# Optimization experiments

Measured on AMD Instinct MI355X. Metric: run time of the kernel, lower is better.

The kernel has to match this reference:

```python
import jax, jax.numpy as jnp
import numpy as np

K = 3
STRIDE = 1


def ste_round(v):
    # Round with straight-through gradient (torch Round Function)
    return v + jax.lax.stop_gradient(jnp.round(v) - v)


def ste_sign(v):
    # Sign with straight-through gradient (torch Sign Function)
    return v + jax.lax.stop_gradient(jnp.sign(v) - v)


def _unfold(x, k, s):
    # torch nn.functional.unfold: [B,C,H,W] -> [B, C*k*k, L], channel-major (c, kh, kw)
    B, C, H, W = x.shape
    Ho = (H - k) // s + 1
    Wo = (W - k) // s + 1
    cols = jnp.stack(
        [x[:, :, i:i + s * Ho:s, j:j + s * Wo:s] for i in range(k) for j in range(k)],
        axis=2,
    )  # [B, C, k*k, Ho, Wo]
    return cols.reshape(B, C * k * k, Ho * Wo)


def reference(x, weight, conv_bias, in_min, in_max, prob_table, rand_idx):
    B = x.shape[0]
    O = weight.shape[0]
    cols = _unfold(x, K, STRIDE)                       # [B, CKK, L]
    CKK = cols.shape[1]
    X = cols.transpose(0, 2, 1).reshape(-1, CKK)       # [N, CKK], N = B*L

    w = ste_sign(weight.reshape(O, CKK))               # ternary weights {-1,0,1}
    wp = jax.nn.relu(w)
    wm = jax.nn.relu(-w)

    scale = in_max - in_min
    Xq = jnp.clip(ste_round((X - in_min) / scale * 15.0), 0.0, 15.0)

    nch = -(-CKK // 4)                                 # ceil(CKK/4)
    pad = nch * 4 - CKK
    if pad:
        Xq = jnp.pad(Xq, ((0, 0), (0, pad)))
        wp = jnp.pad(wp, ((0, 0), (0, pad)))
        wm = jnp.pad(wm, ((0, 0), (0, pad)))

    Xc = Xq.reshape(-1, nch, 4)                        # [N, nch, 4]
    Wp = wp.reshape(O, nch, 4)
    Wm = wm.reshape(O, nch, 4)

    yp = jnp.einsum('nck,ock->cno', Xc, Wp)            # [nch, N, O]
    ym = -jnp.einsum('nck,ock->cno', Xc, Wm)
    T = jnp.stack([yp, ym], axis=1)                    # [nch, 2, N, O]

    longs = jnp.abs(jnp.clip(jnp.round(T), -60.0, 60.0).astype(jnp.int32))
    Q = jnp.clip(ste_round(T / 15.0), -3.0, 3.0)
    temp = prob_table[longs, rand_idx]                 # irregular gather [nch,2,N,O]
    add = temp * jnp.sign(Q) + Q - jax.lax.stop_gradient(Q)

    bias_term = in_min * jnp.sum(w, axis=1)            # linear(InMin*ones, w) -> [O]
    xo = jnp.sum(add, axis=(0, 1)) * scale + bias_term + conv_bias  # [N, O]

    L = X.shape[0] // B
    dim = int(np.sqrt(L))
    return xo.reshape(B, L, O).transpose(0, 2, 1).reshape(B, O, dim, dim)


def setup_inputs() -> dict:
    key = jax.random.key(0)
    k1, k2, k3, k4, k5 = jax.random.split(key, 5)
    B, C, H, W = 2, 16, 66, 66
    O = 64
    CKK = C * K * K            # 144
    nch = -(-CKK // 4)         # 36
    L = ((H - K) // STRIDE + 1) ** 2  # 4096
    N = B * L                  # 8192
    return {
        'x': jax.random.uniform(k1, (B, C, H, W), dtype=jnp.float32),
        'weight': jax.random.normal(k2, (O, C, K, K), dtype=jnp.float32),
        'conv_bias': jax.random.normal(k3, (O,), dtype=jnp.float32),
        'in_min': jnp.zeros((), dtype=jnp.float32),
        'in_max': jnp.ones((), dtype=jnp.float32),
        'prob_table': jax.random.uniform(k4, (61, 1000), dtype=jnp.float32),
        'rand_idx': jax.random.randint(k5, (nch, 2, N, O), 0, 1000, dtype=jnp.int32),
    }
```

## Files before the change

### kernel.cpp

```cpp
#include <hip/hip_runtime.h>

typedef unsigned int uint;

#define B_     2
#define C_     16
#define H_     66
#define W_     66
#define O_     64
#define CKK    144
#define NCH    36
#define DIM    64
#define L_     4096
#define N_     8192
#define PLANE  524288
#define TROWS  61
#define TCOLS  1000

typedef _Float16 h4 __attribute__((ext_vector_type(4)));

__device__ __forceinline__ void loadg(int2 (&buf)[8],
                                      const int* __restrict__ rp, int c0) {
#pragma unroll
    for (int j = 0; j < 4; ++j) {
        int c = c0 + j;
        buf[2 * j + 0] = *(const int2*)(rp + (2 * c)     * PLANE);
        buf[2 * j + 1] = *(const int2*)(rp + (2 * c + 1) * PLANE);
    }
}

__device__ __forceinline__ void procg(const int2 (&buf)[8],
                                      const uint*  __restrict__ xqp,
                                      const uint4* __restrict__ swp,
                                      const _Float16* __restrict__ tbl,
                                      int c0, float& sum0, float& sum1) {
#pragma unroll
    for (int j = 0; j < 4; ++j) {
        int c = c0 + j;
        uint  xv = xqp[c];
        uint4 m  = swp[c * 32];
        uint yp0 = ((xv & m.x) * 0x01010101u) >> 24;
        uint ym0 = ((xv & m.y) * 0x01010101u) >> 24;
        uint yp1 = ((xv & m.z) * 0x01010101u) >> 24;
        uint ym1 = ((xv & m.w) * 0x01010101u) >> 24;
        int2 b0 = buf[2 * j + 0];
        int2 b1 = buf[2 * j + 1];
        sum0 += (float)tbl[yp0 * TCOLS + b0.x];
        sum0 -= (float)tbl[ym0 * TCOLS + b1.x];
        sum1 += (float)tbl[yp1 * TCOLS + b0.y];
        sum1 -= (float)tbl[ym1 * TCOLS + b1.y];
    }
}

__launch_bounds__(1024)
__global__ void k_fused(const float* __restrict__ x,
                        const float* __restrict__ wgt,
                        const float* __restrict__ cbias,
                        const float* __restrict__ pmin,
                        const float* __restrict__ pmax,
                        const float* __restrict__ ptbl,
                        const int*   __restrict__ ridx,
                        float* __restrict__ out) {
    __shared__ __align__(16) _Float16 tbl[TROWS * TCOLS];
    __shared__ uint4 s_w4[NCH * 32];
    __shared__ float s_bias[O_];
    __shared__ uint  s_xq[2][16 * NCH];

    const int tid  = threadIdx.x;
    const int wv   = tid >> 6;
    const int lane = tid & 63;
    const int p    = lane & 31;
    const int h    = lane >> 5;
    const int s    = wv >> 3;
    const int nloc = 2 * (wv & 7) + h;
    const int o0   = 2 * p;

    const float mn = pmin[0];
    const float sc = pmax[0] - mn;

    const int n_g = blockIdx.x * 16 + nloc + s * 4096;
    const int* rp = ridx + n_g * O_ + o0;
    int2 A[8], Bb[8], Cc[8], Dd[8];
    loadg(A,  rp, 0);
    loadg(Bb, rp, 4);
    loadg(Cc, rp, 8);
    loadg(Dd, rp, 12);

    {
        uint4 z; z.x = z.y = z.z = z.w = 0u;
        uint4* zp = (uint4*)tbl;
        for (int q = tid; q < 1000; q += 1024) zp[q] = z;
    }
    {
        const float4* src = (const float4*)(ptbl + 8 * TCOLS);
        h4* dst = (h4*)(tbl + 8 * TCOLS);
        for (int q = tid; q < (53 * TCOLS) / 4; q += 1024) {
            float4 v = src[q];
            h4 hh = { (_Float16)v.x, (_Float16)v.y, (_Float16)v.z, (_Float16)v.w };
            dst[q] = hh;
        }
    }
    for (int q = tid; q < NCH * 32; q += 1024) {
        int c = q >> 5, pp = q & 31;
        uint4 mo;
        float4 v0 = *(const float4*)(wgt + (2 * pp)     * CKK + c * 4);
        float4 v1 = *(const float4*)(wgt + (2 * pp + 1) * CKK + c * 4);
        uint pm = 0, nm = 0;
        if (v0.x > 0.0f) pm |= 0x000000FFu; else if (v0.x < 0.0f) nm |= 0x000000FFu;
        if (v0.y > 0.0f) pm |= 0x0000FF00u; else if (v0.y < 0.0f) nm |= 0x0000FF00u;
        if (v0.z > 0.0f) pm |= 0x00FF0000u; else if (v0.z < 0.0f) nm |= 0x00FF0000u;
        if (v0.w > 0.0f) pm |= 0xFF000000u; else if (v0.w < 0.0f) nm |= 0xFF000000u;
        mo.x = pm; mo.y = nm;
        pm = 0; nm = 0;
        if (v1.x > 0.0f) pm |= 0x000000FFu; else if (v1.x < 0.0f) nm |= 0x000000FFu;
        if (v1.y > 0.0f) pm |= 0x0000FF00u; else if (v1.y < 0.0f) nm |= 0x0000FF00u;
        if (v1.z > 0.0f) pm |= 0x00FF0000u; else if (v1.z < 0.0f) nm |= 0x00FF0000u;
        if (v1.w > 0.0f) pm |= 0xFF000000u; else if (v1.w < 0.0f) nm |= 0xFF000000u;
        mo.z = pm; mo.w = nm;
        s_w4[c * 32 + pp] = mo;
    }
    for (int i = tid; i < 2 * 16 * NCH; i += 1024) {
        int t  = i / (16 * NCH);
        int r  = i - t * (16 * NCH);
        int nl2 = r / NCH;
        int c2  = r - nl2 * NCH;
        int n2  = blockIdx.x * 16 + nl2 + t * 4096;
        int b2 = n2 >> 12, l2 = n2 & (L_ - 1);
        int h2 = l2 >> 6,  w2 = l2 & (DIM - 1);
        uint packed = 0;
#pragma unroll
        for (int k = 0; k < 4; ++k) {
            int j  = c2 * 4 + k;
            int ci = j / 9;
            int r2 = j - ci * 9;
            int kh = r2 / 3;
            int kw = r2 - kh * 3;
            float v = x[((b2 * C_ + ci) * H_ + (h2 + kh)) * W_ + (w2 + kw)];
            float t2 = (v - mn) / sc * 15.0f;
            float q = fminf(fmaxf(rintf(t2), 0.0f), 15.0f);
            packed |= ((uint)q) << (8 * k);
        }
        s_xq[t][r] = packed;
    }
    __syncthreads();

    if (tid < 32) {
        int sw0 = 0, sw1 = 0;
        for (int c = 0; c < NCH; ++c) {
            uint4 m = s_w4[c * 32 + tid];
            sw0 += (__popc(m.x) >> 3) - (__popc(m.y) >> 3);
            sw1 += (__popc(m.z) >> 3) - (__popc(m.w) >> 3);
        }
        s_bias[2 * tid]     = mn * (float)sw0 + cbias[2 * tid];
        s_bias[2 * tid + 1] = mn * (float)sw1 + cbias[2 * tid + 1];
    }
    __syncthreads();

    const uint*  xqp = &s_xq[s][nloc * NCH];
    const uint4* swp = &s_w4[p];
    float sum0 = 0.0f, sum1 = 0.0f;

    procg(A,  xqp, swp, tbl,  0, sum0, sum1); loadg(A,  rp, 16);
    procg(Bb, xqp, swp, tbl,  4, sum0, sum1); loadg(Bb, rp, 20);
    procg(Cc, xqp, swp, tbl,  8, sum0, sum1); loadg(Cc, rp, 24);
    procg(Dd, xqp, swp, tbl, 12, sum0, sum1); loadg(Dd, rp, 28);
    procg(A,  xqp, swp, tbl, 16, sum0, sum1); loadg(A,  rp, 32);
    procg(Bb, xqp, swp, tbl, 20, sum0, sum1);
    procg(Cc, xqp, swp, tbl, 24, sum0, sum1);
    procg(Dd, xqp, swp, tbl, 28, sum0, sum1);
    procg(A,  xqp, swp, tbl, 32, sum0, sum1);

    const int l = blockIdx.x * 16 + nloc;
    out[(s * O_ + o0)     * L_ + l] = sum0 * sc + s_bias[o0];
    out[(s * O_ + o0 + 1) * L_ + l] = sum1 * sc + s_bias[o0 + 1];
}

extern "C" void kernel_launch(void* const* d_in, const int* in_sizes, int n_in,
                              void* d_out, int out_size, void* d_ws, size_t ws_size,
                              hipStream_t stream) {
    const float* x     = (const float*)d_in[0];
    const float* wgt   = (const float*)d_in[1];
    const float* cbias = (const float*)d_in[2];
    const float* pmin  = (const float*)d_in[3];
    const float* pmax  = (const float*)d_in[4];
    const float* ptbl  = (const float*)d_in[5];
    const int*   ridx  = (const int*)d_in[6];
    float* out = (float*)d_out;

    k_fused<<<256, 1024, 0, stream>>>(x, wgt, cbias, pmin, pmax, ptbl, ridx, out);
}
```

Measured before the change: 36.54 us.

## Remap lanes to 4 outputs per sign with int4 loads and padded table

Each lane now handles four consecutive output channels for either the positive or the negative term. It loads rand_idx as int4 (16 bytes) instead of int2, and the two sign halves are combined with a cross-lane shuffle. The fp16 table row stride is padded to 1024 so the gather index becomes a shift instead of a multiply. The bias is now computed directly from the weights, and an extra barrier is added after zeroing the whole enlarged table. The aim is wider global loads and cheaper addressing, at the cost of more shared memory, a shuffle, and half the lanes sitting idle during stores.

```diff
diff --git a/kernel.cpp b/kernel.cpp
--- a/kernel.cpp
+++ b/kernel.cpp
@@ -13,41 +13,38 @@
 #define L_     4096
 #define N_     8192
 #define PLANE  524288
+#define TSTRIDE 1024
 #define TROWS  61
 #define TCOLS  1000
 
 typedef _Float16 h4 __attribute__((ext_vector_type(4)));
 
-__device__ __forceinline__ void loadg(int2 (&buf)[8],
+__device__ __forceinline__ void loadg(int4 (&buf)[4],
                                       const int* __restrict__ rp, int c0) {
 #pragma unroll
-    for (int j = 0; j < 4; ++j) {
-        int c = c0 + j;
-        buf[2 * j + 0] = *(const int2*)(rp + (2 * c)     * PLANE);
-        buf[2 * j + 1] = *(const int2*)(rp + (2 * c + 1) * PLANE);
-    }
+    for (int j = 0; j < 4; ++j)
+        buf[j] = *(const int4*)(rp + (c0 + j) * (2 * PLANE));
 }
 
-__device__ __forceinline__ void procg(const int2 (&buf)[8],
+__device__ __forceinline__ void procg(const int4 (&buf)[4],
                                       const uint*  __restrict__ xqp,
                                       const uint4* __restrict__ swp,
                                       const _Float16* __restrict__ tbl,
-                                      int c0, float& sum0, float& sum1) {
+                                      int c0, float (&sum)[4]) {
 #pragma unroll
     for (int j = 0; j < 4; ++j) {
         int c = c0 + j;
         uint  xv = xqp[c];
         uint4 m  = swp[c * 32];
-        uint yp0 = ((xv & m.x) * 0x01010101u) >> 24;
-        uint ym0 = ((xv & m.y) * 0x01010101u) >> 24;
-        uint yp1 = ((xv & m.z) * 0x01010101u) >> 24;
-        uint ym1 = ((xv & m.w) * 0x01010101u) >> 24;
-        int2 b0 = buf[2 * j + 0];
-        int2 b1 = buf[2 * j + 1];
-        sum0 += (float)tbl[yp0 * TCOLS + b0.x];
-        sum0 -= (float)tbl[ym0 * TCOLS + b1.x];
-        sum1 += (float)tbl[yp1 * TCOLS + b0.y];
-        sum1 -= (float)tbl[ym1 * TCOLS + b1.y];
+        int4  ix = buf[j];
+        uint r0 = ((xv & m.x) * 0x01010101u) >> 24;
+        uint r1 = ((xv & m.y) * 0x01010101u) >> 24;
+        uint r2 = ((xv & m.z) * 0x01010101u) >> 24;
+        uint r3 = ((xv & m.w) * 0x01010101u) >> 24;
+        sum[0] += (float)tbl[(r0 << 10) + ix.x];
+        sum[1] += (float)tbl[(r1 << 10) + ix.y];
+        sum[2] += (float)tbl[(r2 << 10) + ix.z];
+        sum[3] += (float)tbl[(r3 << 10) + ix.w];
     }
 }
 
@@ -60,26 +57,26 @@
                         const float* __restrict__ ptbl,
                         const int*   __restrict__ ridx,
                         float* __restrict__ out) {
-    __shared__ __align__(16) _Float16 tbl[TROWS * TCOLS];
-    __shared__ uint4 s_w4[NCH * 32];
+    __shared__ __align__(16) _Float16 tbl[TROWS * TSTRIDE];
+    __shared__ uint4 s_wq[NCH * 2 * 16];
     __shared__ float s_bias[O_];
     __shared__ uint  s_xq[2][16 * NCH];
 
     const int tid  = threadIdx.x;
     const int wv   = tid >> 6;
     const int lane = tid & 63;
-    const int p    = lane & 31;
-    const int h    = lane >> 5;
-    const int s    = wv >> 3;
-    const int nloc = 2 * (wv & 7) + h;
-    const int o0   = 2 * p;
+    const int quad = lane & 15;
+    const int sg   = (lane >> 4) & 1;
+    const int nsub = lane >> 5;
+    const int t    = wv >> 3;
+    const int nloc = 2 * (wv & 7) + nsub;
 
     const float mn = pmin[0];
     const float sc = pmax[0] - mn;
 
-    const int n_g = blockIdx.x * 16 + nloc + s * 4096;
-    const int* rp = ridx + n_g * O_ + o0;
-    int2 A[8], Bb[8], Cc[8], Dd[8];
+    const int n_g = blockIdx.x * 16 + nloc + t * 4096;
+    const int* rp = ridx + sg * PLANE + n_g * O_ + quad * 4;
+    int4 A[4], Bb[4], Cc[4], Dd[4];
     loadg(A,  rp, 0);
     loadg(Bb, rp, 4);
     loadg(Cc, rp, 8);
@@ -88,42 +85,39 @@
     {
         uint4 z; z.x = z.y = z.z = z.w = 0u;
         uint4* zp = (uint4*)tbl;
-        for (int q = tid; q < 1000; q += 1024) zp[q] = z;
+        for (int q = tid; q < (TROWS * TSTRIDE) / 8; q += 1024) zp[q] = z;
     }
-    {
-        const float4* src = (const float4*)(ptbl + 8 * TCOLS);
-        h4* dst = (h4*)(tbl + 8 * TCOLS);
-        for (int q = tid; q < (53 * TCOLS) / 4; q += 1024) {
-            float4 v = src[q];
-            h4 hh = { (_Float16)v.x, (_Float16)v.y, (_Float16)v.z, (_Float16)v.w };
-            dst[q] = hh;
-        }
+    __syncthreads();
+    for (int q = tid; q < 53 * 250; q += 1024) {
+        int r = q / 250, k = q - r * 250;
+        float4 v = *(const float4*)(ptbl + (8 + r) * TCOLS + k * 4);
+        h4 hh = { (_Float16)v.x, (_Float16)v.y, (_Float16)v.z, (_Float16)v.w };
+        *(h4*)(tbl + (8 + r) * TSTRIDE + k * 4) = hh;
     }
     for (int q = tid; q < NCH * 32; q += 1024) {
-        int c = q >> 5, pp = q & 31;
+        int c = q >> 5, r = q & 31;
+        int sgg = r >> 4, qd = r & 15;
         uint4 mo;
-        float4 v0 = *(const float4*)(wgt + (2 * pp)     * CKK + c * 4);
-        float4 v1 = *(const float4*)(wgt + (2 * pp + 1) * CKK + c * 4);
-        uint pm = 0, nm = 0;
-        if (v0.x > 0.0f) pm |= 0x000000FFu; else if (v0.x < 0.0f) nm |= 0x000000FFu;
-        if (v0.y > 0.0f) pm |= 0x0000FF00u; else if (v0.y < 0.0f) nm |= 0x0000FF00u;
-        if (v0.z > 0.0f) pm |= 0x00FF0000u; else if (v0.z < 0.0f) nm |= 0x00FF0000u;
-        if (v0.w > 0.0f) pm |= 0xFF000000u; else if (v0.w < 0.0f) nm |= 0xFF000000u;
-        mo.x = pm; mo.y = nm;
-        pm = 0; nm = 0;
-        if (v1.x > 0.0f) pm |= 0x000000FFu; else if (v1.x < 0.0f) nm |= 0x000000FFu;
-        if (v1.y > 0.0f) pm |= 0x0000FF00u; else if (v1.y < 0.0f) nm |= 0x0000FF00u;
-        if (v1.z > 0.0f) pm |= 0x00FF0000u; else if (v1.z < 0.0f) nm |= 0x00FF0000u;
-        if (v1.w > 0.0f) pm |= 0xFF000000u; else if (v1.w < 0.0f) nm |= 0xFF000000u;
-        mo.z = pm; mo.w = nm;
-        s_w4[c * 32 + pp] = mo;
+        uint mk[4];
+#pragma unroll
+        for (int j = 0; j < 4; ++j) {
+            float4 v = *(const float4*)(wgt + (4 * qd + j) * CKK + c * 4);
+            uint pm = 0, nm = 0;
+            if (v.x > 0.0f) pm |= 0x000000FFu; else if (v.x < 0.0f) nm |= 0x000000FFu;
+            if (v.y > 0.0f) pm |= 0x0000FF00u; else if (v.y < 0.0f) nm |= 0x0000FF00u;
+            if (v.z > 0.0f) pm |= 0x00FF0000u; else if (v.z < 0.0f) nm |= 0x00FF0000u;
+            if (v.w > 0.0f) pm |= 0xFF000000u; else if (v.w < 0.0f) nm |= 0xFF000000u;
+            mk[j] = sgg ? nm : pm;
+        }
+        mo.x = mk[0]; mo.y = mk[1]; mo.z = mk[2]; mo.w = mk[3];
+        s_wq[(c * 2 + sgg) * 16 + qd] = mo;
     }
     for (int i = tid; i < 2 * 16 * NCH; i += 1024) {
-        int t  = i / (16 * NCH);
-        int r  = i - t * (16 * NCH);
+        int tt = i / (16 * NCH);
+        int r  = i - tt * (16 * NCH);
         int nl2 = r / NCH;
         int c2  = r - nl2 * NCH;
-        int n2  = blockIdx.x * 16 + nl2 + t * 4096;
+        int n2  = blockIdx.x * 16 + nl2 + tt * 4096;
         int b2 = n2 >> 12, l2 = n2 & (L_ - 1);
         int h2 = l2 >> 6,  w2 = l2 & (DIM - 1);
         uint packed = 0;
@@ -139,39 +133,46 @@
             float q = fminf(fmaxf(rintf(t2), 0.0f), 15.0f);
             packed |= ((uint)q) << (8 * k);
         }
-        s_xq[t][r] = packed;
+        s_xq[tt][r] = packed;
+    }
+    if (tid < O_) {
+        int sw = 0;
+        for (int j = 0; j < CKK; ++j) {
+            float v = wgt[tid * CKK + j];
+            sw += (v > 0.0f) - (v < 0.0f);
+        }
+        s_bias[tid] = mn * (float)sw + cbias[tid];
     }
     __syncthreads();
 
-    if (tid < 32) {
-        int sw0 = 0, sw1 = 0;
-        for (int c = 0; c < NCH; ++c) {
-            uint4 m = s_w4[c * 32 + tid];
-            sw0 += (__popc(m.x) >> 3) - (__popc(m.y) >> 3);
-            sw1 += (__popc(m.z) >> 3) - (__popc(m.w) >> 3);
-        }
-        s_bias[2 * tid]     = mn * (float)sw0 + cbias[2 * tid];
-        s_bias[2 * tid + 1] = mn * (float)sw1 + cbias[2 * tid + 1];
+    const uint*  xqp = &s_xq[t][nloc * NCH];
+    const uint4* swp = &s_wq[sg * 16 + quad];
+    float sum[4] = {0.f, 0.f, 0.f, 0.f};
+
+    procg(A,  xqp, swp, tbl,  0, sum); loadg(A,  rp, 16);
+    procg(Bb, xqp, swp, tbl,  4, sum); loadg(Bb, rp, 20);
+    procg(Cc, xqp, swp, tbl,  8, sum); loadg(Cc, rp, 24);
+    procg(Dd, xqp, swp, tbl, 12, sum); loadg(Dd, rp, 28);
+    procg(A,  xqp, swp, tbl, 16, sum); loadg(A,  rp, 32);
+    procg(Bb, xqp, swp, tbl, 20, sum);
+    procg(Cc, xqp, swp, tbl, 24, sum);
+    procg(Dd, xqp, swp, tbl, 28, sum);
+    procg(A,  xqp, swp, tbl, 32, sum);
+
+    float f0 = sum[0] - __shfl_xor(sum[0], 16, 64);
+    float f1 = sum[1] - __shfl_xor(sum[1], 16, 64);
+    float f2 = sum[2] - __shfl_xor(sum[2], 16, 64);
+    float f3 = sum[3] - __shfl_xor(sum[3], 16, 64);
+
+    if (sg == 0) {
+        const int l  = blockIdx.x * 16 + nloc;
+        const int o0 = 4 * quad;
+        float4 bv = *(const float4*)(s_bias + o0);
+        out[(t * O_ + o0 + 0) * L_ + l] = f0 * sc + bv.x;
+        out[(t * O_ + o0 + 1) * L_ + l] = f1 * sc + bv.y;
+        out[(t * O_ + o0 + 2) * L_ + l] = f2 * sc + bv.z;
+        out[(t * O_ + o0 + 3) * L_ + l] = f3 * sc + bv.w;
     }
-    __syncthreads();
-
-    const uint*  xqp = &s_xq[s][nloc * NCH];
-    const uint4* swp = &s_w4[p];
-    float sum0 = 0.0f, sum1 = 0.0f;
-
-    procg(A,  xqp, swp, tbl,  0, sum0, sum1); loadg(A,  rp, 16);
-    procg(Bb, xqp, swp, tbl,  4, sum0, sum1); loadg(Bb, rp, 20);
-    procg(Cc, xqp, swp, tbl,  8, sum0, sum1); loadg(Cc, rp, 24);
-    procg(Dd, xqp, swp, tbl, 12, sum0, sum1); loadg(Dd, rp, 28);
-    procg(A,  xqp, swp, tbl, 16, sum0, sum1); loadg(A,  rp, 32);
-    procg(Bb, xqp, swp, tbl, 20, sum0, sum1);
-    procg(Cc, xqp, swp, tbl, 24, sum0, sum1);
-    procg(Dd, xqp, swp, tbl, 28, sum0, sum1);
-    procg(A,  xqp, swp, tbl, 32, sum0, sum1);
-
-    const int l = blockIdx.x * 16 + nloc;
-    out[(s * O_ + o0)     * L_ + l] = sum0 * sc + s_bias[o0];
-    out[(s * O_ + o0 + 1) * L_ + l] = sum1 * sc + s_bias[o0 + 1];
 }
 
 extern "C" void kernel_launch(void* const* d_in, const int* in_sizes, int n_in,
```

New measurement: 40.88 us. +11.9%, slower.
